# Kernel tuning notes

Measured on AMD Instinct MI355X. Metric: run time of the kernel, lower is better.

Reference implementation:

```python
import jax, jax.numpy as jnp
import numpy as np

EPS_NORM = 1e-6
EPS_Q = 1e-5


def rmsnorm(x, g):
    var = jnp.mean(jnp.square(x), axis=-1, keepdims=True)
    return x * jax.lax.rsqrt(var + EPS_NORM) * g


def act_quant(x):
    # per-token int8 absmax fake-quant (BitNet)
    scale = 127.0 / jnp.clip(jnp.max(jnp.abs(x), axis=-1, keepdims=True), EPS_Q, None)
    return jnp.clip(jnp.round(x * scale), -128.0, 127.0) / scale


def weight_quant(w):
    # per-tensor ternary (b1.58) fake-quant
    scale = 1.0 / jnp.clip(jnp.mean(jnp.abs(w)), EPS_Q, None)
    return jnp.clip(jnp.round(w * scale), -1.0, 1.0) / scale


def ste(x, fn):
    return x + jax.lax.stop_gradient(fn(x) - x)


def bitlinear(x, w, g):
    # RMSNorm -> act fake-quant (STE) -> ternary weight fake-quant (STE) -> matmul
    xn = rmsnorm(x, g)
    xq = ste(xn, act_quant)
    wq = ste(w, weight_quant)
    return jnp.einsum('bsd,od->bso', xq, wq)


def setup_inputs() -> dict:
    key = jax.random.key(0)
    k1, k2, k3 = jax.random.split(key, 3)
    B, S, D, I = 4, 4096, 2048, 5632
    x = jax.random.normal(k1, (B, S, D), dtype=jnp.float32)
    w_gate = jax.random.normal(k2, (2 * I, D), dtype=jnp.float32) * (D ** -0.5)
    g_gate = jnp.ones((D,), dtype=jnp.float32)
    w_down = jax.random.normal(k3, (D, I), dtype=jnp.float32) * (I ** -0.5)
    g_down = jnp.ones((I,), dtype=jnp.float32)
    return {"x": x, "w_gate": w_gate, "g_gate": g_gate,
            "w_down": w_down, "g_down": g_down}


def reference(x, w_gate, g_gate, w_down, g_down):
    y = bitlinear(x, w_gate, g_gate)            # [B, S, 2*I]
    gate, v = jnp.split(y, 2, axis=-1)          # chunk(2, -1)
    swiglu_out = gate * jax.nn.sigmoid(gate) * v  # swish(gate) * v
    z = bitlinear(swiglu_out, w_down, g_down)   # [B, S, D]
    return z
```

## Files before the change

### kernel.cpp

```cpp
#include <hip/hip_runtime.h>
#include <hip/hip_bf16.h>

typedef int v4i __attribute__((ext_vector_type(4)));

#define DEV __device__ __forceinline__

DEV void gload16(const void* g, void* l){
  __builtin_amdgcn_global_load_lds((const __attribute__((address_space(1))) unsigned int*)g,
                                   (__attribute__((address_space(3))) unsigned int*)l, 16, 0, 0);
}

DEV float block_sum256(float v, float* red){
#pragma unroll
  for (int o=32;o>0;o>>=1) v += __shfl_down(v,o);
  int w = threadIdx.x>>6;
  if ((threadIdx.x&63)==0) red[w]=v;
  __syncthreads();
  v = red[0]+red[1]+red[2]+red[3];
  __syncthreads();
  return v;
}
DEV float block_max256(float v, float* red){
#pragma unroll
  for (int o=32;o>0;o>>=1) v = fmaxf(v,__shfl_down(v,o));
  int w = threadIdx.x>>6;
  if ((threadIdx.x&63)==0) red[w]=v;
  __syncthreads();
  v = fmaxf(fmaxf(red[0],red[1]),fmaxf(red[2],red[3]));
  __syncthreads();
  return v;
}

__global__ __launch_bounds__(256) void reduce_abs_kernel(const float* __restrict__ w, long n4,
                                                         float* __restrict__ partials){
  __shared__ float red[4];
  const float4* w4 = (const float4*)w;
  float s = 0.f;
  for (long i = (long)blockIdx.x*256 + threadIdx.x; i < n4; i += (long)gridDim.x*256){
    float4 v = w4[i];
    s += fabsf(v.x)+fabsf(v.y)+fabsf(v.z)+fabsf(v.w);
  }
  s = block_sum256(s, red);
  if (threadIdx.x==0) partials[blockIdx.x]=s;
}

__global__ __launch_bounds__(256) void finalize_scales_kernel(const float* __restrict__ partials,
                                                              float* __restrict__ hdr){
  __shared__ float red[4];
  float s1=0.f, s2=0.f;
  for (int i=threadIdx.x;i<1024;i+=256){ s1+=partials[i]; s2+=partials[i+1024]; }
  s1 = block_sum256(s1, red);
  s2 = block_sum256(s2, red);
  if (threadIdx.x==0){
    float m1 = s1 / 23068672.0f;
    float sc1 = 1.0f / fmaxf(m1, 1e-5f);
    hdr[0]=sc1; hdr[1]=1.0f/sc1;
    float m2 = s2 / 11534336.0f;
    float sc2 = 1.0f / fmaxf(m2, 1e-5f);
    hdr[2]=sc2; hdr[3]=1.0f/sc2;
  }
}

__global__ __launch_bounds__(256) void quant_w_kernel(const float* __restrict__ w,
                                                      signed char* __restrict__ wq, long n4,
                                                      const float* __restrict__ hdr, int hi){
  float scale = hdr[hi];
  const float4* w4 = (const float4*)w;
  unsigned* o4 = (unsigned*)wq;
  for (long i = (long)blockIdx.x*256 + threadIdx.x; i < n4; i += (long)gridDim.x*256){
    float4 v = w4[i];
    int q0 = (int)fminf(fmaxf(rintf(v.x*scale),-1.f),1.f);
    int q1 = (int)fminf(fmaxf(rintf(v.y*scale),-1.f),1.f);
    int q2 = (int)fminf(fmaxf(rintf(v.z*scale),-1.f),1.f);
    int q3 = (int)fminf(fmaxf(rintf(v.w*scale),-1.f),1.f);
    unsigned pk = (q0&0xff) | ((q1&0xff)<<8) | ((q2&0xff)<<16) | ((q3&0xff)<<24);
    o4[i] = pk;
  }
}

__global__ __launch_bounds__(256) void rms_quant_x_kernel(const float* __restrict__ x,
                                                          const float* __restrict__ g,
                                                          signed char* __restrict__ xq,
                                                          float* __restrict__ isx){
  __shared__ float red[4];
  const int row = blockIdx.x, t = threadIdx.x;
  const float* xr = x + (size_t)row*2048 + t*8;
  float4 a = *(const float4*)xr;
  float4 b = *(const float4*)(xr+4);
  float xv[8] = {a.x,a.y,a.z,a.w,b.x,b.y,b.z,b.w};
  float ss = 0.f;
#pragma unroll
  for (int i=0;i<8;i++) ss += xv[i]*xv[i];
  ss = block_sum256(ss, red);
  float rs = rsqrtf(ss*(1.0f/2048.0f) + 1e-6f);
  const float* gr = g + t*8;
  float4 ga = *(const float4*)gr;
  float4 gb = *(const float4*)(gr+4);
  float gv[8] = {ga.x,ga.y,ga.z,ga.w,gb.x,gb.y,gb.z,gb.w};
  float xn[8]; float m = 0.f;
#pragma unroll
  for (int i=0;i<8;i++){ xn[i] = xv[i]*rs*gv[i]; m = fmaxf(m, fabsf(xn[i])); }
  m = block_max256(m, red);
  float scale = 127.0f / fmaxf(m, 1e-5f);
  unsigned long long pk = 0;
#pragma unroll
  for (int i=0;i<8;i++){
    int q = (int)fminf(fmaxf(rintf(xn[i]*scale), -128.0f), 127.0f);
    pk |= (unsigned long long)(unsigned char)(signed char)q << (8*i);
  }
  *(unsigned long long*)(xq + (size_t)row*2048 + t*8) = pk;
  if (t==0) isx[row] = 1.0f/scale;
}

__global__ __launch_bounds__(256) void rms_quant_sg_kernel(const __hip_bfloat16* __restrict__ sg,
                                                           const float* __restrict__ g,
                                                           signed char* __restrict__ xq,
                                                           float* __restrict__ isx){
  __shared__ float red[4];
  const int row = blockIdx.x, t = threadIdx.x;
  const unsigned* sr = (const unsigned*)(sg + (size_t)row*5632);
  float s[22];
  float ss = 0.f;
#pragma unroll
  for (int i=0;i<11;i++){
    unsigned u = sr[t + i*256];
    float f0 = __uint_as_float(u<<16);
    float f1 = __uint_as_float(u & 0xffff0000u);
    s[2*i]=f0; s[2*i+1]=f1;
    ss += f0*f0 + f1*f1;
  }
  ss = block_sum256(ss, red);
  float rs = rsqrtf(ss*(1.0f/5632.0f) + 1e-6f);
  const float2* g2 = (const float2*)g;
  float xn[22]; float m = 0.f;
#pragma unroll
  for (int i=0;i<11;i++){
    float2 gv = g2[t + i*256];
    xn[2*i]   = s[2*i]  *rs*gv.x;
    xn[2*i+1] = s[2*i+1]*rs*gv.y;
    m = fmaxf(m, fmaxf(fabsf(xn[2*i]), fabsf(xn[2*i+1])));
  }
  m = block_max256(m, red);
  float scale = 127.0f / fmaxf(m, 1e-5f);
  short* o2 = (short*)(xq + (size_t)row*5632);
#pragma unroll
  for (int i=0;i<11;i++){
    int q0 = (int)fminf(fmaxf(rintf(xn[2*i]  *scale), -128.0f), 127.0f);
    int q1 = (int)fminf(fmaxf(rintf(xn[2*i+1]*scale), -128.0f), 127.0f);
    o2[t + i*256] = (short)((q0 & 0xff) | ((q1 & 0xff) << 8));
  }
  if (t==0) isx[row] = 1.0f/scale;
}

__global__ __launch_bounds__(512) void gemm1_swiglu_kernel(const signed char* __restrict__ A,
                                                           const signed char* __restrict__ B,
                                                           const float* __restrict__ inv_sx,
                                                           const float* __restrict__ hdr,
                                                           __hip_bfloat16* __restrict__ out){
  constexpr int K = 2048;
  constexpr int NI = 5632;
  constexpr int NT = 16;
  __shared__ __align__(16) unsigned char smem[131072];

  const int t = threadIdx.x;
  const int lid = blockIdx.x + blockIdx.y * gridDim.x;
  const int nid = (lid & 7) * 352 + (lid >> 3);
  const int bm0 = (nid / 44) * 256;
  const int bc0 = (nid % 44) * 128;
  const int w = t >> 6, l = t & 63;
  const int ts = w >> 2;
  const int wv = w & 3;
  const int wr = wv * 64;
  const int lr = l & 15, lg = l >> 4;

  const float inv_sw = hdr[1];

  const signed char* aSrc[4]; int aOff[4];
#pragma unroll
  for (int i=0;i<4;i++){
    int c = t + i*512; int r = c>>3, k = c&7;
    aSrc[i] = A + (size_t)(bm0 + r)*K + (k ^ (r&7))*16;
    aOff[i] = c*16;
  }
  const signed char* bSrc[4]; int bOff[4];
#pragma unroll
  for (int i=0;i<4;i++){
    int c = t + i*512; int tile = c>>10, r = (c>>3)&127, k = c&7;
    int grow = (tile ? NI : 0) + bc0 + r;
    bSrc[i] = B + (size_t)grow*K + (k ^ (r&7))*16;
    bOff[i] = 32768 + c*16;
  }

  v4i acc[4][8] = {};

#define STAGE1(BUF, KT) do{ unsigned char* _bb = smem + (BUF)*65536;              \
  _Pragma("unroll") for (int _i=0;_i<4;_i++) gload16(aSrc[_i] + (KT)*128, _bb + aOff[_i]); \
  _Pragma("unroll") for (int _i=0;_i<4;_i++) gload16(bSrc[_i] + (KT)*128, _bb + bOff[_i]); }while(0)

#define COMP1(BUF) do{                                                            \
  const signed char* _As = (const signed char*)smem + (BUF)*65536;                \
  const signed char* _Bs = _As + 32768;                                           \
  _Pragma("unroll") for (int kk=0;kk<2;++kk){                                     \
    v4i af[4], bf[8];                                                             \
    _Pragma("unroll") for (int i=0;i<4;i++){                                      \
      int row = wr + i*16 + lr;                                                   \
      af[i] = *(const v4i*)(_As + row*128 + (((kk*4+lg) ^ (row&7))*16));          \
    }                                                                             \
    _Pragma("unroll") for (int j=0;j<8;j++){                                      \
      int row = j*16 + lr;                                                        \
      bf[j] = *(const v4i*)(_Bs + ts*16384 + row*128 + (((kk*4+lg) ^ (row&7))*16));\
    }                                                                             \
    __builtin_amdgcn_s_setprio(1);                                                \
    _Pragma("unroll") for (int j=0;j<8;j++)                                       \
      _Pragma("unroll") for (int i=0;i<4;i++)                                     \
        acc[i][j] = __builtin_amdgcn_mfma_i32_16x16x64_i8(af[i], bf[j], acc[i][j], 0, 0, 0); \
    __builtin_amdgcn_s_setprio(0);                                                \
  } }while(0)

  STAGE1(0, 0);
  STAGE1(1, 1);
  for (int kt = 0; kt < NT-2; kt += 2){
    asm volatile("s_waitcnt vmcnt(8)" ::: "memory");
    __builtin_amdgcn_s_barrier();
    __builtin_amdgcn_sched_barrier(0);
    COMP1(0);
    __builtin_amdgcn_sched_barrier(0);
    __builtin_amdgcn_s_barrier();
    STAGE1(0, kt+2);
    asm volatile("s_waitcnt vmcnt(8)" ::: "memory");
    __builtin_amdgcn_s_barrier();
    __builtin_amdgcn_sched_barrier(0);
    COMP1(1);
    __builtin_amdgcn_sched_barrier(0);
    __builtin_amdgcn_s_barrier();
    STAGE1(1, kt+3);
  }
  asm volatile("s_waitcnt vmcnt(8)" ::: "memory");
  __builtin_amdgcn_s_barrier();
  __builtin_amdgcn_sched_barrier(0);
  COMP1(0);
  __builtin_amdgcn_sched_barrier(0);
  __builtin_amdgcn_s_barrier();
  asm volatile("s_waitcnt vmcnt(0)" ::: "memory");
  __builtin_amdgcn_s_barrier();
  __builtin_amdgcn_sched_barrier(0);
  COMP1(1);
  __builtin_amdgcn_sched_barrier(0);

  float* vex = (float*)smem;
  __syncthreads();
  if (ts == 1){
#pragma unroll
    for (int i=0;i<4;i++){
#pragma unroll
      for (int r=0;r<4;r++){
        int lrow = wr + i*16 + lg*4 + r;
        float f = inv_sx[bm0 + lrow] * inv_sw;
#pragma unroll
        for (int j=0;j<8;j++)
          vex[lrow*128 + j*16 + lr] = (float)acc[i][j][r] * f;
      }
    }
  }
  __syncthreads();
  if (ts == 0){
#pragma unroll
    for (int i=0;i<4;i++){
#pragma unroll
      for (int r=0;r<4;r++){
        int lrow = wr + i*16 + lg*4 + r;
        float f = inv_sx[bm0 + lrow] * inv_sw;
#pragma unroll
        for (int j=0;j<8;j++){
          float gv = (float)acc[i][j][r] * f;
          float vv = vex[lrow*128 + j*16 + lr];
          float sw = gv / (1.0f + expf(-gv)) * vv;
          acc[i][j][r] = __float_as_int(sw);
        }
      }
    }
  }
  __syncthreads();
  __hip_bfloat16* obuf = (__hip_bfloat16*)smem;
  if (ts == 0){
#pragma unroll
    for (int i=0;i<4;i++){
#pragma unroll
      for (int r=0;r<4;r++){
        int lrow = wr + i*16 + lg*4 + r;
#pragma unroll
        for (int j=0;j<8;j++)
          obuf[lrow*128 + j*16 + lr] = __float2bfloat16(__int_as_float(acc[i][j][r]));
      }
    }
  }
  __syncthreads();
#pragma unroll
  for (int it=0; it<8; ++it){
    int idx = t + it*512;
    int row = idx >> 4, c16 = idx & 15;
    *(int4*)((char*)(out + (size_t)(bm0+row)*NI + bc0) + c16*16) =
        *(const int4*)((const char*)obuf + row*256 + c16*16);
  }
#undef STAGE1
#undef COMP1
}

__global__ __launch_bounds__(256) void gemm2_kernel(const signed char* __restrict__ A,
                                                    const signed char* __restrict__ B,
                                                    const float* __restrict__ inv_sx,
                                                    const float* __restrict__ hdr,
                                                    float* __restrict__ out){
  constexpr int K = 5632;
  constexpr int N = 2048;
  constexpr int NT = 44;
  __shared__ __align__(16) unsigned char smem[65536];

  const int t = threadIdx.x;
  const int lid = blockIdx.x + blockIdx.y * gridDim.x;
  const int nid = (lid & 7) * 256 + (lid >> 3);
  const int bm0 = (nid >> 4) * 128;
  const int bn0 = (nid & 15) * 128;
  const int w = t >> 6, l = t & 63;
  const int wr = (w >> 1) * 64, wc = (w & 1) * 64;
  const int lr = l & 15, lg = l >> 4;

  const float inv_sw = hdr[3];

  const signed char *aSrc[4], *bSrc[4]; int aOff[4], bOff[4];
#pragma unroll
  for (int i=0;i<4;i++){
    int c = t + i*256; int r = c>>3, k = c&7;
    aSrc[i] = A + (size_t)(bm0 + r)*K + (k ^ (r&7))*16;
    bSrc[i] = B + (size_t)(bn0 + r)*K + (k ^ (r&7))*16;
    aOff[i] = c*16;
    bOff[i] = 16384 + c*16;
  }

  v4i acc[4][4] = {};

#define STAGE2(BUF, KT) do{ unsigned char* _bb = smem + (BUF)*32768;              \
  _Pragma("unroll") for (int _i=0;_i<4;_i++){                                     \
    gload16(aSrc[_i] + (KT)*128, _bb + aOff[_i]);                                 \
    gload16(bSrc[_i] + (KT)*128, _bb + bOff[_i]); } }while(0)

#define COMP2(BUF) do{                                                            \
  const signed char* _As = (const signed char*)smem + (BUF)*32768;                \
  const signed char* _Bs = _As + 16384;                                           \
  _Pragma("unroll") for (int kk=0;kk<2;++kk){                                     \
    v4i af[4], bf[4];                                                             \
    _Pragma("unroll") for (int i=0;i<4;i++){                                      \
      int row = wr + i*16 + lr;                                                   \
      af[i] = *(const v4i*)(_As + row*128 + (((kk*4+lg) ^ (row&7))*16));          \
    }                                                                             \
    _Pragma("unroll") for (int j=0;j<4;j++){                                      \
      int row = wc + j*16 + lr;                                                   \
      bf[j] = *(const v4i*)(_Bs + row*128 + (((kk*4+lg) ^ (row&7))*16));          \
    }                                                                             \
    __builtin_amdgcn_s_setprio(1);                                                \
    _Pragma("unroll") for (int i=0;i<4;i++)                                       \
      _Pragma("unroll") for (int j=0;j<4;j++)                                     \
        acc[i][j] = __builtin_amdgcn_mfma_i32_16x16x64_i8(af[i], bf[j], acc[i][j], 0, 0, 0); \
    __builtin_amdgcn_s_setprio(0);                                                \
  } }while(0)

  STAGE2(0, 0);
  STAGE2(1, 1);
  for (int kt = 0; kt < NT-2; kt += 2){
    asm volatile("s_waitcnt vmcnt(8)" ::: "memory");
    __builtin_amdgcn_s_barrier();
    __builtin_amdgcn_sched_barrier(0);
    COMP2(0);
    __builtin_amdgcn_sched_barrier(0);
    __builtin_amdgcn_s_barrier();
    STAGE2(0, kt+2);
    asm volatile("s_waitcnt vmcnt(8)" ::: "memory");
    __builtin_amdgcn_s_barrier();
    __builtin_amdgcn_sched_barrier(0);
    COMP2(1);
    __builtin_amdgcn_sched_barrier(0);
    __builtin_amdgcn_s_barrier();
    STAGE2(1, kt+3);
  }
  asm volatile("s_waitcnt vmcnt(8)" ::: "memory");
  __builtin_amdgcn_s_barrier();
  __builtin_amdgcn_sched_barrier(0);
  COMP2(0);
  __builtin_amdgcn_sched_barrier(0);
  __builtin_amdgcn_s_barrier();
  asm volatile("s_waitcnt vmcnt(0)" ::: "memory");
  __builtin_amdgcn_s_barrier();
  __builtin_amdgcn_sched_barrier(0);
  COMP2(1);
  __builtin_amdgcn_sched_barrier(0);

#pragma unroll
  for (int i=0;i<4;i++){
#pragma unroll
    for (int r=0;r<4;r++){
      int lrow = wr + i*16 + lg*4 + r;
      float f = inv_sx[bm0 + lrow] * inv_sw;
      size_t o = (size_t)(bm0 + lrow) * N + bn0;
#pragma unroll
      for (int j=0;j<4;j++)
        out[o + wc + j*16 + lr] = (float)acc[i][j][r] * f;
    }
  }
#undef STAGE2
#undef COMP2
}

extern "C" void kernel_launch(void* const* d_in, const int* in_sizes, int n_in,
                              void* d_out, int out_size, void* d_ws, size_t ws_size,
                              hipStream_t stream) {
  const float* x      = (const float*)d_in[0];
  const float* w_gate = (const float*)d_in[1];
  const float* g_gate = (const float*)d_in[2];
  const float* w_down = (const float*)d_in[3];
  const float* g_down = (const float*)d_in[4];
  float* out = (float*)d_out;

  char* p = (char*)d_ws;
  float* hdr      = (float*)p;
  float* partials = (float*)(p + 64);
  size_t off = 8448;
  signed char* wqg = (signed char*)(p + off); off += 23068672;
  signed char* wqd = (signed char*)(p + off); off += 11534336;
  signed char* xq1 = (signed char*)(p + off); off += 33554432;
  signed char* xq2 = (signed char*)(p + off); off += 92274688;
  float* isx1 = (float*)(p + off); off += 65536;
  float* isx2 = (float*)(p + off); off += 65536;
  __hip_bfloat16* sg = (__hip_bfloat16*)(p + off); off += 184549376;

  reduce_abs_kernel<<<1024,256,0,stream>>>(w_gate, 23068672/4, partials);
  reduce_abs_kernel<<<1024,256,0,stream>>>(w_down, 11534336/4, partials+1024);
  finalize_scales_kernel<<<1,256,0,stream>>>(partials, hdr);
  quant_w_kernel<<<2048,256,0,stream>>>(w_gate, wqg, 23068672/4, hdr, 0);
  quant_w_kernel<<<1024,256,0,stream>>>(w_down, wqd, 11534336/4, hdr, 2);
  rms_quant_x_kernel<<<16384,256,0,stream>>>(x, g_gate, xq1, isx1);
  gemm1_swiglu_kernel<<<dim3(44,64),512,0,stream>>>(xq1, wqg, isx1, hdr, sg);
  rms_quant_sg_kernel<<<16384,256,0,stream>>>(sg, g_down, xq2, isx2);
  gemm2_kernel<<<dim3(16,128),256,0,stream>>>(xq2, wqd, isx2, hdr, out);
}
```

Before: 829.1 us.

## Use 4-stage BK=64 pipeline in gemm1 and swizzle tile order for L2 locality

Gemm1 moves from a double-buffered 128-wide K tile to a four-buffer ring of 64-wide K tiles. Three tiles are prefetched, and each step does one barrier instead of two. LDS addresses are precomputed and use a new XOR swizzle for 64-byte rows. Both GEMMs also remap block IDs so each XCD handles a compact grouped patch of output tiles, aiming for better L2 reuse of A and B. The risks are the waitcnt accounting across ring slots and the hazard from dropping the post-compute barrier before restaging.

Measured after the change: 871.9 us. +5.2%, slower.

```diff
diff --git a/kernel.cpp b/kernel.cpp
--- a/kernel.cpp
+++ b/kernel.cpp
@@ -159,14 +159,17 @@
                                                            __hip_bfloat16* __restrict__ out){
   constexpr int K = 2048;
   constexpr int NI = 5632;
-  constexpr int NT = 16;
+  constexpr int NT = 32;
   __shared__ __align__(16) unsigned char smem[131072];
 
   const int t = threadIdx.x;
   const int lid = blockIdx.x + blockIdx.y * gridDim.x;
-  const int nid = (lid & 7) * 352 + (lid >> 3);
-  const int bm0 = (nid / 44) * 256;
-  const int bc0 = (nid % 44) * 128;
+  const int xc = lid & 7;
+  const int sx = lid >> 3;
+  const int ch = sx >> 5;
+  const int ii = sx & 31;
+  const int bm0 = (xc*8 + (ii>>2)) * 256;
+  const int bc0 = (ch*4 + (ii&3)) * 128;
   const int w = t >> 6, l = t & 63;
   const int ts = w >> 2;
   const int wv = w & 3;
@@ -175,76 +178,67 @@
 
   const float inv_sw = hdr[1];
 
-  const signed char* aSrc[4]; int aOff[4];
-#pragma unroll
-  for (int i=0;i<4;i++){
-    int c = t + i*512; int r = c>>3, k = c&7;
-    aSrc[i] = A + (size_t)(bm0 + r)*K + (k ^ (r&7))*16;
+  const signed char* aSrc[2]; int aOff[2];
+#pragma unroll
+  for (int i=0;i<2;i++){
+    int c = t + i*512, r = c>>2, kp = c&3;
+    aSrc[i] = A + (size_t)(bm0 + r)*K + ((kp ^ ((r>>1)&3))*16);
     aOff[i] = c*16;
   }
-  const signed char* bSrc[4]; int bOff[4];
-#pragma unroll
-  for (int i=0;i<4;i++){
-    int c = t + i*512; int tile = c>>10, r = (c>>3)&127, k = c&7;
-    int grow = (tile ? NI : 0) + bc0 + r;
-    bSrc[i] = B + (size_t)grow*K + (k ^ (r&7))*16;
-    bOff[i] = 32768 + c*16;
-  }
+  const signed char* bSrc[2]; int bOff[2];
+#pragma unroll
+  for (int i=0;i<2;i++){
+    int c = t + i*512, r = c>>2, kp = c&3;
+    int grow = ((r>>7) ? NI : 0) + bc0 + (r&127);
+    bSrc[i] = B + (size_t)grow*K + ((kp ^ ((r>>1)&3))*16);
+    bOff[i] = 16384 + c*16;
+  }
+  int aoff[4];
+#pragma unroll
+  for (int i=0;i<4;i++){ int row = wr + i*16 + lr; aoff[i] = row*64 + ((lg ^ ((row>>1)&3))*16); }
+  int boff[8];
+#pragma unroll
+  for (int j=0;j<8;j++){ int row = ts*128 + j*16 + lr; boff[j] = 16384 + row*64 + ((lg ^ ((row>>1)&3))*16); }
 
   v4i acc[4][8] = {};
 
-#define STAGE1(BUF, KT) do{ unsigned char* _bb = smem + (BUF)*65536;              \
-  _Pragma("unroll") for (int _i=0;_i<4;_i++) gload16(aSrc[_i] + (KT)*128, _bb + aOff[_i]); \
-  _Pragma("unroll") for (int _i=0;_i<4;_i++) gload16(bSrc[_i] + (KT)*128, _bb + bOff[_i]); }while(0)
-
-#define COMP1(BUF) do{                                                            \
-  const signed char* _As = (const signed char*)smem + (BUF)*65536;                \
-  const signed char* _Bs = _As + 32768;                                           \
-  _Pragma("unroll") for (int kk=0;kk<2;++kk){                                     \
-    v4i af[4], bf[8];                                                             \
-    _Pragma("unroll") for (int i=0;i<4;i++){                                      \
-      int row = wr + i*16 + lr;                                                   \
-      af[i] = *(const v4i*)(_As + row*128 + (((kk*4+lg) ^ (row&7))*16));          \
-    }                                                                             \
-    _Pragma("unroll") for (int j=0;j<8;j++){                                      \
-      int row = j*16 + lr;                                                        \
-      bf[j] = *(const v4i*)(_Bs + ts*16384 + row*128 + (((kk*4+lg) ^ (row&7))*16));\
-    }                                                                             \
-    __builtin_amdgcn_s_setprio(1);                                                \
-    _Pragma("unroll") for (int j=0;j<8;j++)                                       \
-      _Pragma("unroll") for (int i=0;i<4;i++)                                     \
-        acc[i][j] = __builtin_amdgcn_mfma_i32_16x16x64_i8(af[i], bf[j], acc[i][j], 0, 0, 0); \
-    __builtin_amdgcn_s_setprio(0);                                                \
-  } }while(0)
-
-  STAGE1(0, 0);
-  STAGE1(1, 1);
-  for (int kt = 0; kt < NT-2; kt += 2){
+#define STAGE1(BUF, KT) { unsigned char* _b = smem + (BUF)*32768;      \
+    gload16(aSrc[0] + (KT)*64, _b + aOff[0]);                          \
+    gload16(aSrc[1] + (KT)*64, _b + aOff[1]);                          \
+    gload16(bSrc[0] + (KT)*64, _b + bOff[0]);                          \
+    gload16(bSrc[1] + (KT)*64, _b + bOff[1]); }
+
+#define COMP1(BUF) {                                                   \
+  const signed char* _bs = (const signed char*)smem + (BUF)*32768;     \
+  v4i af[4], bf[8];                                                    \
+  _Pragma("unroll") for (int _i=0;_i<4;_i++) af[_i] = *(const v4i*)(_bs + aoff[_i]); \
+  _Pragma("unroll") for (int _j=0;_j<8;_j++) bf[_j] = *(const v4i*)(_bs + boff[_j]); \
+  __builtin_amdgcn_s_setprio(1);                                       \
+  _Pragma("unroll") for (int _j=0;_j<8;_j++)                           \
+    _Pragma("unroll") for (int _i=0;_i<4;_i++)                         \
+      acc[_i][_j] = __builtin_amdgcn_mfma_i32_16x16x64_i8(af[_i], bf[_j], acc[_i][_j], 0, 0, 0); \
+  __builtin_amdgcn_s_setprio(0);                                       \
+}
+
+  STAGE1(0,0); STAGE1(1,1); STAGE1(2,2);
+
+  for (int kt = 0; kt < NT-2; ++kt){
     asm volatile("s_waitcnt vmcnt(8)" ::: "memory");
     __builtin_amdgcn_s_barrier();
     __builtin_amdgcn_sched_barrier(0);
-    COMP1(0);
-    __builtin_amdgcn_sched_barrier(0);
-    __builtin_amdgcn_s_barrier();
-    STAGE1(0, kt+2);
-    asm volatile("s_waitcnt vmcnt(8)" ::: "memory");
-    __builtin_amdgcn_s_barrier();
-    __builtin_amdgcn_sched_barrier(0);
-    COMP1(1);
-    __builtin_amdgcn_sched_barrier(0);
-    __builtin_amdgcn_s_barrier();
-    STAGE1(1, kt+3);
-  }
-  asm volatile("s_waitcnt vmcnt(8)" ::: "memory");
+    COMP1(kt&3);
+    __builtin_amdgcn_sched_barrier(0);
+    if (kt <= NT-4) STAGE1((kt+3)&3, kt+3);
+  }
+  asm volatile("s_waitcnt vmcnt(4)" ::: "memory");
   __builtin_amdgcn_s_barrier();
   __builtin_amdgcn_sched_barrier(0);
-  COMP1(0);
-  __builtin_amdgcn_sched_barrier(0);
-  __builtin_amdgcn_s_barrier();
+  COMP1((NT-2)&3);
+  __builtin_amdgcn_sched_barrier(0);
   asm volatile("s_waitcnt vmcnt(0)" ::: "memory");
   __builtin_amdgcn_s_barrier();
   __builtin_amdgcn_sched_barrier(0);
-  COMP1(1);
+  COMP1((NT-1)&3);
   __builtin_amdgcn_sched_barrier(0);
 
   float* vex = (float*)smem;
@@ -318,9 +312,11 @@
 
   const int t = threadIdx.x;
   const int lid = blockIdx.x + blockIdx.y * gridDim.x;
-  const int nid = (lid & 7) * 256 + (lid >> 3);
-  const int bm0 = (nid >> 4) * 128;
-  const int bn0 = (nid & 15) * 128;
+  const int xc = lid & 7;
+  const int sx = lid >> 3;
+  const int ch = sx >> 4, ii = sx & 15;
+  const int bm0 = (xc*16 + (ch>>2)*4 + (ii>>2)) * 128;
+  const int bn0 = ((ch&3)*4 + (ii&3)) * 128;
   const int w = t >> 6, l = t & 63;
   const int wr = (w >> 1) * 64, wc = (w & 1) * 64;
   const int lr = l & 15, lg = l >> 4;
@@ -330,11 +326,11 @@
   const signed char *aSrc[4], *bSrc[4]; int aOff[4], bOff[4];
 #pragma unroll
   for (int i=0;i<4;i++){
-    int c = t + i*256; int r = c>>3, k = c&7;
-    aSrc[i] = A + (size_t)(bm0 + r)*K + (k ^ (r&7))*16;
-    bSrc[i] = B + (size_t)(bn0 + r)*K + (k ^ (r&7))*16;
-    aOff[i] = c*16;
-    bOff[i] = 16384 + c*16;
+    int cc = t + i*256; int r = cc>>3, k = cc&7;
+    aSrc[i] = A + (size_t)(bm0 + r)*K + ((k ^ (r&7))*16);
+    bSrc[i] = B + (size_t)(bn0 + r)*K + ((k ^ (r&7))*16);
+    aOff[i] = cc*16;
+    bOff[i] = 16384 + cc*16;
   }
 
   v4i acc[4][4] = {};
```
